# Performance work log

Measured on AMD Instinct MI355X. Metric: run time of the kernel, lower is better.

Reference implementation:

```python
import jax, jax.numpy as jnp
import numpy as np

B, T, D, H = 2, 2048, 1024, 16
HD = D // H  # head_dim = 64

def setup_inputs() -> dict:
    key = jax.random.key(0)
    ks = jax.random.split(key, 6)
    s = 1.0 / np.sqrt(D)
    return {
        "x": jax.random.normal(ks[0], (B, T, D), jnp.float32),
        "Wq": jax.random.normal(ks[1], (D, D), jnp.float32) * s,
        "Wk": jax.random.normal(ks[2], (D, D), jnp.float32) * s,
        "Wv": jax.random.normal(ks[3], (D, D), jnp.float32) * s,
        "Wo": jax.random.normal(ks[4], (D, D), jnp.float32) * s,
        "bo": jnp.zeros((D,), jnp.float32),
    }

def reference(x, Wq, Wk, Wv, Wo, bo):
    b, n, _ = x.shape
    # projections -> [b, h, n, hd]
    def split_heads(t):
        return t.reshape(b, n, H, HD).transpose(0, 2, 1, 3)
    q = split_heads(x @ Wq)
    k = split_heads(x @ Wk)
    v = split_heads(x @ Wv)
    scale = HD ** 0.5
    scores = jnp.einsum('bhqd,bhkd->bhqk', q, k) / scale
    causal = jnp.tril(jnp.ones((n, n), bool))  # True = keep
    scores = jnp.where(causal, scores, -jnp.inf)
    attn = jax.nn.softmax(scores, axis=-1)
    ctx = jnp.einsum('bhqk,bhkd->bhqd', attn, v)
    ctx = ctx.transpose(0, 2, 1, 3).reshape(b, n, D)
    return ctx @ Wo + bo
```

## Files before the change

kernel.cpp:

```cpp
#include <hip/hip_runtime.h>
#include <stdint.h>

typedef unsigned short u16;
typedef unsigned int   u32;
typedef __attribute__((ext_vector_type(8))) __bf16 bf8;
typedef __attribute__((ext_vector_type(4))) float  f4;

#define NEG_INF (-__builtin_inff())

#define BB 2
#define TT 2048
#define DD 1024
#define HH 16
#define HD 64
#define BT (BB*TT)

#define SBAR() __builtin_amdgcn_s_barrier()
#define VMCNT4() asm volatile("s_waitcnt vmcnt(4)" ::: "memory")
#define VMCNT0() asm volatile("s_waitcnt vmcnt(0)" ::: "memory")
#define LGKMCNT0() asm volatile("s_waitcnt lgkmcnt(0)" ::: "memory")

__device__ __forceinline__ u16 f2bf(float f) {
  u32 u = __builtin_bit_cast(u32, f);
  u += 0x7FFFu + ((u >> 16) & 1u);
  return (u16)(u >> 16);
}

__device__ __forceinline__ float exp2fast(float x) {
  float r; asm("v_exp_f32 %0, %1" : "=v"(r) : "v"(x)); return r;
}

__device__ __forceinline__ void g2l16(const void* g, void* l) {
  __builtin_amdgcn_global_load_lds((const __attribute__((address_space(1))) u32*)g,
                                   (__attribute__((address_space(3))) u32*)l, 16, 0, 0);
}

__global__ void k_cast_x(const float* __restrict__ x, uint4* __restrict__ xb) {
  int i = blockIdx.x * 256 + threadIdx.x;
  const float4* xf = (const float4*)x;
  float4 a = xf[2*i], b = xf[2*i+1];
  uint4 o;
  o.x = (u32)f2bf(a.x) | ((u32)f2bf(a.y) << 16);
  o.y = (u32)f2bf(a.z) | ((u32)f2bf(a.w) << 16);
  o.z = (u32)f2bf(b.x) | ((u32)f2bf(b.y) << 16);
  o.w = (u32)f2bf(b.z) | ((u32)f2bf(b.w) << 16);
  xb[i] = o;
}

__global__ void k_twcast(const float* __restrict__ w0, const float* __restrict__ w1,
                         const float* __restrict__ w2, const float* __restrict__ w3,
                         u16* __restrict__ o0, u16* __restrict__ o1,
                         u16* __restrict__ o2, u16* __restrict__ o3) {
  const float* W; u16* O;
  switch (blockIdx.z) {
    case 0: W = w0; O = o0; break;
    case 1: W = w1; O = o1; break;
    case 2: W = w2; O = o2; break;
    default: W = w3; O = o3; break;
  }
  __shared__ __align__(16) u16 tile[64][80];
  int tid = threadIdx.x;
  int k0 = blockIdx.y * 64, n0 = blockIdx.x * 64;
#pragma unroll
  for (int it = 0; it < 4; ++it) {
    int c = it*256 + tid; int kr = c >> 4, ns = c & 15;
    float4 v = *(const float4*)(W + (size_t)(k0+kr)*DD + n0 + ns*4);
    u16* p = &tile[kr][ns*4];
    p[0] = f2bf(v.x); p[1] = f2bf(v.y); p[2] = f2bf(v.z); p[3] = f2bf(v.w);
  }
  __syncthreads();
#pragma unroll
  for (int it = 0; it < 2; ++it) {
    int c = it*256 + tid; int nr = c >> 3, ks = c & 7;
    u32 ww[4];
#pragma unroll
    for (int e = 0; e < 4; ++e) {
      u16 lo = tile[ks*8 + 2*e][nr], hi = tile[ks*8 + 2*e + 1][nr];
      ww[e] = (u32)lo | ((u32)hi << 16);
    }
    uint4 o; o.x = ww[0]; o.y = ww[1]; o.z = ww[2]; o.w = ww[3];
    *(uint4*)(O + (size_t)(n0+nr)*DD + k0 + ks*8) = o;
  }
}

__global__ __launch_bounds__(256, 2) void k_qkv(const u16* __restrict__ xb,
    const u16* __restrict__ wqt, const u16* __restrict__ wkt, const u16* __restrict__ wvt,
    u16* __restrict__ qo, u16* __restrict__ ko, u16* __restrict__ vo) {
  __shared__ __align__(16) char smem[32768];
  int tid = threadIdx.x, w = tid >> 6, l = tid & 63;
  int bid = blockIdx.y * 24 + blockIdx.x;
  int wg = (bid & 7) * 96 + (bid >> 3);
  int nb = wg % 24, mb = wg / 24;
  const u16* Bt = (nb < 8) ? wqt : (nb < 16 ? wkt : wvt);
  int nbl = nb & 7;
  int wm = w >> 1, wn = w & 1;
  f4 z = {0.f, 0.f, 0.f, 0.f};
  f4 acc[4][4];
#pragma unroll
  for (int i = 0; i < 4; ++i)
#pragma unroll
    for (int j = 0; j < 4; ++j) acc[i][j] = z;

  auto stage = [&](int buf, int kt) {
    int kk = kt * 32;
    char* dst = smem + buf * 16384;
#pragma unroll
    for (int i = 0; i < 2; ++i) {
      int c = i*256 + tid; int row = c >> 2, u = c & 3, s = u ^ ((row >> 1) & 3);
      g2l16(xb + (size_t)(mb*128 + row)*DD + kk + s*8, dst + (i*256 + w*64)*16);
    }
#pragma unroll
    for (int i = 0; i < 2; ++i) {
      int c = i*256 + tid; int row = c >> 2, u = c & 3, s = u ^ ((row >> 1) & 3);
      g2l16(Bt + (size_t)(nbl*128 + row)*DD + kk + s*8, dst + 8192 + (i*256 + w*64)*16);
    }
  };

  stage(0, 0);
  VMCNT0(); SBAR();
#pragma unroll 2
  for (int kt = 0; kt < 32; ++kt) {
    int cur = kt & 1;
    if (kt < 31) stage(cur ^ 1, kt + 1);
    char* buf = smem + cur * 16384;
    bf8 af[4], bfr[4];
#pragma unroll
    for (int mf = 0; mf < 4; ++mf) {
      int row = wm*64 + mf*16 + (l & 15);
      int s = (l >> 4) ^ ((row >> 1) & 3);
      af[mf] = *(const bf8*)(buf + row*64 + s*16);
    }
#pragma unroll
    for (int nf = 0; nf < 4; ++nf) {
      int row = wn*64 + nf*16 + (l & 15);
      int s = (l >> 4) ^ ((row >> 1) & 3);
      bfr[nf] = *(const bf8*)(buf + 8192 + row*64 + s*16);
    }
    __builtin_amdgcn_s_setprio(1);
#pragma unroll
    for (int mf = 0; mf < 4; ++mf)
#pragma unroll
      for (int nf = 0; nf < 4; ++nf)
        acc[mf][nf] = __builtin_amdgcn_mfma_f32_16x16x32_bf16(af[mf], bfr[nf], acc[mf][nf], 0, 0, 0);
    __builtin_amdgcn_s_setprio(0);
    LGKMCNT0();
    VMCNT0(); SBAR();
  }
  if (nb < 16) {
    u16* Out = (nb < 8) ? qo : ko;
    float qs = (nb < 8) ? 0.18033688011112042f : 1.0f;
#pragma unroll
    for (int mf = 0; mf < 4; ++mf) {
      int m0 = mb*128 + wm*64 + mf*16 + (l >> 4)*4;
      int b = m0 >> 11;
#pragma unroll
      for (int nf = 0; nf < 4; ++nf) {
        int nn = nbl*128 + wn*64 + nf*16 + (l & 15);
        int h = nn >> 6, d = nn & 63;
#pragma unroll
        for (int r = 0; r < 4; ++r) {
          int t = (m0 + r) & 2047;
          Out[(size_t)((b*HH + h)*TT + t)*HD + d] = f2bf(acc[mf][nf][r] * qs);
        }
      }
    }
  } else {
#pragma unroll
    for (int mf = 0; mf < 4; ++mf) {
      int m0 = mb*128 + wm*64 + mf*16 + (l >> 4)*4;
      int b = m0 >> 11, t0 = m0 & 2047;
#pragma unroll
      for (int nf = 0; nf < 4; ++nf) {
        int nn = nbl*128 + wn*64 + nf*16 + (l & 15);
        int h = nn >> 6, d = nn & 63;
        uint2 o;
        o.x = (u32)f2bf(acc[mf][nf][0]) | ((u32)f2bf(acc[mf][nf][1]) << 16);
        o.y = (u32)f2bf(acc[mf][nf][2]) | ((u32)f2bf(acc[mf][nf][3]) << 16);
        *(uint2*)(vo + (size_t)((b*HH + h)*HD + d)*TT + t0) = o;
      }
    }
  }
}

__global__ __launch_bounds__(256, 2) void k_attn(const u16* __restrict__ q,
    const u16* __restrict__ kk, const u16* __restrict__ vt, u16* __restrict__ ctx) {
  __shared__ __align__(16) char smem[50176];
  int tid = threadIdx.x, w = tid >> 6, l = tid & 63;
  int qi = l & 15, g = l >> 4;
  int fid = blockIdx.x;
  int xcd = fid & 7, j = fid >> 3;
  int bh  = xcd * 4 + (j & 3);
  int ip  = j >> 2;
  u32* Pw = (u32*)(smem + 32768) + w * 1088;
  int b = bh >> 4, h = bh & 15;
  int rot2 = 2 * (qi & 7);

  auto stageK = [&](int t) {
#pragma unroll
    for (int i = 0; i < 4; ++i) {
      int c = i*256 + tid; int row = c >> 3, u = c & 7;
      g2l16(kk + (size_t)(bh*TT + t*128 + row)*HD + (u ^ (row & 7))*8,
            smem + (i*256 + w*64)*16);
    }
  };
  auto stageV = [&](int t) {
#pragma unroll
    for (int i = 0; i < 4; ++i) {
      int c = i*256 + tid; int row = c >> 4, u = c & 15;
      g2l16(vt + (size_t)(bh*HD + row)*TT + t*128 + (u ^ (row & 15))*8,
            smem + 16384 + (i*256 + w*64)*16);
    }
  };

  for (int ps = 0; ps < 2; ++ps) {
    int q0 = (ps ? (31 - ip) : ip) * 64;
    int qw = q0 + w * 16;
    int qrow = qw + qi;
    const u16* qbase = q + (size_t)(bh*TT + qrow)*HD + g*8;
    bf8 qf0 = *(const bf8*)(qbase);
    bf8 qf1 = *(const bf8*)(qbase + 32);
    float mreg = NEG_INF, lreg = 0.f;
    f4 z = {0.f, 0.f, 0.f, 0.f};
    f4 acc[4]; acc[0] = z; acc[1] = z; acc[2] = z; acc[3] = z;
    int nt = (q0 >> 7) + 1;
    stageK(0); stageV(0);
    for (int t = 0; t < nt; ++t) {
      bool last = (t == nt - 1);
      VMCNT4();
      SBAR();
      __builtin_amdgcn_s_setprio(1);
      f4 sv[8];
#pragma unroll
      for (int jf = 0; jf < 8; ++jf) {
        f4 s = z;
        int row = jf*16 + qi;
        int s0 = g ^ (row & 7);
        int s1 = (g + 4) ^ (row & 7);
        bf8 b0 = *(const bf8*)(smem + row*128 + s0*16);
        bf8 b1 = *(const bf8*)(smem + row*128 + s1*16);
        s = __builtin_amdgcn_mfma_f32_16x16x32_bf16(b0, qf0, s, 0, 0, 0);
        s = __builtin_amdgcn_mfma_f32_16x16x32_bf16(b1, qf1, s, 0, 0, 0);
        sv[jf] = s;
      }
      __builtin_amdgcn_s_setprio(0);
      LGKMCNT0();
      SBAR();
      if (!last) stageK(t + 1);
      if (t*128 + 127 > qw) {
        int cbase = qrow - t*128 - 4*g;
#pragma unroll
        for (int jf = 0; jf < 8; ++jf)
#pragma unroll
          for (int r = 0; r < 4; ++r)
            if (jf*16 + r > cbase) sv[jf][r] = NEG_INF;
      }
      float mx = NEG_INF;
#pragma unroll
      for (int jf = 0; jf < 8; ++jf)
        mx = fmaxf(mx, fmaxf(fmaxf(sv[jf][0], sv[jf][1]), fmaxf(sv[jf][2], sv[jf][3])));
      mx = fmaxf(mx, __shfl_xor(mx, 16, 64));
      mx = fmaxf(mx, __shfl_xor(mx, 32, 64));
      float mnew = fmaxf(mreg, mx);
      float alpha = exp2fast(mreg - mnew);
      mreg = mnew;
      float rs = 0.f;
#pragma unroll
      for (int jf = 0; jf < 8; ++jf) {
        float p0 = exp2fast(sv[jf][0] - mreg);
        float p1 = exp2fast(sv[jf][1] - mreg);
        float p2 = exp2fast(sv[jf][2] - mreg);
        float p3 = exp2fast(sv[jf][3] - mreg);
        rs += (p0 + p1) + (p2 + p3);
        uint2 pv;
        pv.x = (u32)f2bf(p0) | ((u32)f2bf(p1) << 16);
        pv.y = (u32)f2bf(p2) | ((u32)f2bf(p3) << 16);
        int blk = 2*jf + (g >> 1);
        *(uint2*)(&Pw[qi*68 + 4*((blk + rot2) & 15) + 2*(g & 1)]) = pv;
      }
      rs += __shfl_xor(rs, 16, 64);
      rs += __shfl_xor(rs, 32, 64);
      lreg = lreg * alpha + rs;
#pragma unroll
      for (int df = 0; df < 4; ++df) {
        f4 a = acc[df];
        a[0] *= alpha; a[1] *= alpha; a[2] *= alpha; a[3] *= alpha;
        acc[df] = a;
      }
      if (!last) { VMCNT4(); } else { VMCNT0(); }
      SBAR();
      __builtin_amdgcn_s_setprio(1);
#pragma unroll
      for (int ks = 0; ks < 4; ++ks) {
        bf8 pf = *(const bf8*)(&Pw[qi*68 + 4*(((4*ks + g) + rot2) & 15)]);
#pragma unroll
        for (int df = 0; df < 4; ++df) {
          int row = df*16 + qi;
          int sl = (ks*4 + g) ^ (row & 15);
          bf8 vf = *(const bf8*)(smem + 16384 + row*256 + sl*16);
          acc[df] = __builtin_amdgcn_mfma_f32_16x16x32_bf16(vf, pf, acc[df], 0, 0, 0);
        }
      }
      __builtin_amdgcn_s_setprio(0);
      LGKMCNT0();
      SBAR();
      if (!last) stageV(t + 1);
    }
    float inv = 1.0f / lreg;
    u16* dst = ctx + (size_t)(b*TT + qrow)*DD + h*HD;
#pragma unroll
    for (int df = 0; df < 4; ++df) {
      uint2 o;
      o.x = (u32)f2bf(acc[df][0] * inv) | ((u32)f2bf(acc[df][1] * inv) << 16);
      o.y = (u32)f2bf(acc[df][2] * inv) | ((u32)f2bf(acc[df][3] * inv) << 16);
      *(uint2*)(dst + df*16 + 4*g) = o;
    }
  }
}

__global__ __launch_bounds__(256, 2) void k_out(const u16* __restrict__ ctx,
    const u16* __restrict__ wot, const float* __restrict__ bo, float* __restrict__ out) {
  __shared__ __align__(16) char smem[24576];
  int tid = threadIdx.x, w = tid >> 6, l = tid & 63;
  int bid = blockIdx.x;
  int wg = (bid & 7) * 64 + (bid >> 3);
  int nb = wg % 16, mb = wg / 16;
  int wm = w >> 1, wn = w & 1;
  f4 z = {0.f, 0.f, 0.f, 0.f};
  f4 acc[4][2];
#pragma unroll
  for (int i = 0; i < 4; ++i) { acc[i][0] = z; acc[i][1] = z; }

  auto stage = [&](int buf, int kt) {
    int kk = kt * 32;
    char* dst = smem + buf * 12288;
#pragma unroll
    for (int i = 0; i < 2; ++i) {
      int c = i*256 + tid; int row = c >> 2, u = c & 3, s = u ^ ((row >> 1) & 3);
      g2l16(ctx + (size_t)(mb*128 + row)*DD + kk + s*8, dst + (i*256 + w*64)*16);
    }
    {
      int row = tid >> 2, u = tid & 3, s = u ^ ((row >> 1) & 3);
      g2l16(wot + (size_t)(nb*64 + row)*DD + kk + s*8, dst + 8192 + (w*64)*16);
    }
  };

  stage(0, 0);
  VMCNT0(); SBAR();
#pragma unroll 2
  for (int kt = 0; kt < 32; ++kt) {
    int cur = kt & 1;
    if (kt < 31) stage(cur ^ 1, kt + 1);
    char* buf = smem + cur * 12288;
    bf8 af[4], bfr[2];
#pragma unroll
    for (int mf = 0; mf < 4; ++mf) {
      int row = wm*64 + mf*16 + (l & 15);
      int s = (l >> 4) ^ ((row >> 1) & 3);
      af[mf] = *(const bf8*)(buf + row*64 + s*16);
    }
#pragma unroll
    for (int nf = 0; nf < 2; ++nf) {
      int row = wn*32 + nf*16 + (l & 15);
      int s = (l >> 4) ^ ((row >> 1) & 3);
      bfr[nf] = *(const bf8*)(buf + 8192 + row*64 + s*16);
    }
    __builtin_amdgcn_s_setprio(1);
#pragma unroll
    for (int mf = 0; mf < 4; ++mf)
#pragma unroll
      for (int nf = 0; nf < 2; ++nf)
        acc[mf][nf] = __builtin_amdgcn_mfma_f32_16x16x32_bf16(af[mf], bfr[nf], acc[mf][nf], 0, 0, 0);
    __builtin_amdgcn_s_setprio(0);
    LGKMCNT0();
    VMCNT0(); SBAR();
  }
#pragma unroll
  for (int nf = 0; nf < 2; ++nf) {
    int n = nb*64 + wn*32 + nf*16 + (l & 15);
    float bias = bo[n];
#pragma unroll
    for (int mf = 0; mf < 4; ++mf) {
      int m0 = mb*128 + wm*64 + mf*16 + (l >> 4)*4;
#pragma unroll
      for (int r = 0; r < 4; ++r)
        out[(size_t)(m0 + r)*DD + n] = acc[mf][nf][r] + bias;
    }
  }
}

extern "C" void kernel_launch(void* const* d_in, const int* in_sizes, int n_in,
                              void* d_out, int out_size, void* d_ws, size_t ws_size,
                              hipStream_t stream) {
  const float* x  = (const float*)d_in[0];
  const float* Wq = (const float*)d_in[1];
  const float* Wk = (const float*)d_in[2];
  const float* Wv = (const float*)d_in[3];
  const float* Wo = (const float*)d_in[4];
  const float* bo = (const float*)d_in[5];
  float* out = (float*)d_out;
  char* ws = (char*)d_ws;

  u16* xb  = (u16*)(ws);
  u16* wqt = (u16*)(ws + 8388608);
  u16* wkt = (u16*)(ws + 10485760);
  u16* wvt = (u16*)(ws + 12582912);
  u16* wot = (u16*)(ws + 14680064);
  u16* qb_ = (u16*)(ws + 16777216);
  u16* kb_ = (u16*)(ws + 25165824);
  u16* vtb = (u16*)(ws + 41943040);
  u16* cxb = (u16*)(ws + 50331648);

  k_cast_x<<<dim3(2048), dim3(256), 0, stream>>>(x, (uint4*)xb);
  k_twcast<<<dim3(16, 16, 4), dim3(256), 0, stream>>>(Wq, Wk, Wv, Wo, wqt, wkt, wvt, wot);
  k_qkv<<<dim3(24, 32), dim3(256), 0, stream>>>(xb, wqt, wkt, wvt, qb_, kb_, vtb);
  k_attn<<<dim3(512), dim3(256), 0, stream>>>(qb_, kb_, vtb, cxb);
  k_out<<<dim3(512), dim3(256), 0, stream>>>(cxb, wot, bo, out);
}
```

Measured before the change: 174.7 us.

## Double GEMM K-tile depth, add lazy softmax rescaling, use hardware bf16 packing

The QKV and output-projection GEMMs now stage 64-wide K tiles instead of 32, with a matching 8-way XOR swizzle and twice the shared memory. This halves the number of barrier and wait cycles per tile. The attention kernel skips the running-max rescale of the accumulator and row sum unless some lane's new max exceeds the old one by more than 8 (log2 units), which saves exp and multiply work but lets unnormalised values grow by up to 2^8. Manual bf16 rounding is replaced by a compiler bf16 conversion for P and the context output. The larger LDS footprint may reduce occupancy in the GEMM kernels.

```diff
diff --git a/kernel.cpp b/kernel.cpp
--- a/kernel.cpp
+++ b/kernel.cpp
@@ -4,6 +4,7 @@
 typedef unsigned short u16;
 typedef unsigned int   u32;
 typedef __attribute__((ext_vector_type(8))) __bf16 bf8;
+typedef __attribute__((ext_vector_type(2))) __bf16 bf2;
 typedef __attribute__((ext_vector_type(4))) float  f4;
 
 #define NEG_INF (-__builtin_inff())
@@ -24,6 +25,11 @@
   u32 u = __builtin_bit_cast(u32, f);
   u += 0x7FFFu + ((u >> 16) & 1u);
   return (u16)(u >> 16);
+}
+
+__device__ __forceinline__ u32 pkbf(float a, float b) {
+  bf2 v; v[0] = (__bf16)a; v[1] = (__bf16)b;
+  return __builtin_bit_cast(u32, v);
 }
 
 __device__ __forceinline__ float exp2fast(float x) {
@@ -86,7 +92,7 @@
 __global__ __launch_bounds__(256, 2) void k_qkv(const u16* __restrict__ xb,
     const u16* __restrict__ wqt, const u16* __restrict__ wkt, const u16* __restrict__ wvt,
     u16* __restrict__ qo, u16* __restrict__ ko, u16* __restrict__ vo) {
-  __shared__ __align__(16) char smem[32768];
+  __shared__ __align__(16) char smem[65536];
   int tid = threadIdx.x, w = tid >> 6, l = tid & 63;
   int bid = blockIdx.y * 24 + blockIdx.x;
   int wg = (bid & 7) * 96 + (bid >> 3);
@@ -94,6 +100,7 @@
   const u16* Bt = (nb < 8) ? wqt : (nb < 16 ? wkt : wvt);
   int nbl = nb & 7;
   int wm = w >> 1, wn = w & 1;
+  int qi = l & 15, g = l >> 4;
   f4 z = {0.f, 0.f, 0.f, 0.f};
   f4 acc[4][4];
 #pragma unroll
@@ -102,47 +109,50 @@
     for (int j = 0; j < 4; ++j) acc[i][j] = z;
 
   auto stage = [&](int buf, int kt) {
-    int kk = kt * 32;
-    char* dst = smem + buf * 16384;
-#pragma unroll
-    for (int i = 0; i < 2; ++i) {
-      int c = i*256 + tid; int row = c >> 2, u = c & 3, s = u ^ ((row >> 1) & 3);
+    int kk = kt * 64;
+    char* dst = smem + buf * 32768;
+#pragma unroll
+    for (int i = 0; i < 4; ++i) {
+      int c = i*256 + tid; int row = c >> 3, u = c & 7, s = u ^ (row & 7);
       g2l16(xb + (size_t)(mb*128 + row)*DD + kk + s*8, dst + (i*256 + w*64)*16);
     }
 #pragma unroll
-    for (int i = 0; i < 2; ++i) {
-      int c = i*256 + tid; int row = c >> 2, u = c & 3, s = u ^ ((row >> 1) & 3);
-      g2l16(Bt + (size_t)(nbl*128 + row)*DD + kk + s*8, dst + 8192 + (i*256 + w*64)*16);
+    for (int i = 0; i < 4; ++i) {
+      int c = i*256 + tid; int row = c >> 3, u = c & 7, s = u ^ (row & 7);
+      g2l16(Bt + (size_t)(nbl*128 + row)*DD + kk + s*8, dst + 16384 + (i*256 + w*64)*16);
     }
   };
 
   stage(0, 0);
   VMCNT0(); SBAR();
 #pragma unroll 2
-  for (int kt = 0; kt < 32; ++kt) {
+  for (int kt = 0; kt < 16; ++kt) {
     int cur = kt & 1;
-    if (kt < 31) stage(cur ^ 1, kt + 1);
-    char* buf = smem + cur * 16384;
-    bf8 af[4], bfr[4];
-#pragma unroll
-    for (int mf = 0; mf < 4; ++mf) {
-      int row = wm*64 + mf*16 + (l & 15);
-      int s = (l >> 4) ^ ((row >> 1) & 3);
-      af[mf] = *(const bf8*)(buf + row*64 + s*16);
-    }
-#pragma unroll
-    for (int nf = 0; nf < 4; ++nf) {
-      int row = wn*64 + nf*16 + (l & 15);
-      int s = (l >> 4) ^ ((row >> 1) & 3);
-      bfr[nf] = *(const bf8*)(buf + 8192 + row*64 + s*16);
-    }
-    __builtin_amdgcn_s_setprio(1);
-#pragma unroll
-    for (int mf = 0; mf < 4; ++mf)
-#pragma unroll
-      for (int nf = 0; nf < 4; ++nf)
-        acc[mf][nf] = __builtin_amdgcn_mfma_f32_16x16x32_bf16(af[mf], bfr[nf], acc[mf][nf], 0, 0, 0);
-    __builtin_amdgcn_s_setprio(0);
+    if (kt < 15) stage(cur ^ 1, kt + 1);
+    char* buf = smem + cur * 32768;
+#pragma unroll
+    for (int ks2 = 0; ks2 < 2; ++ks2) {
+      bf8 af[4], bfr[4];
+#pragma unroll
+      for (int mf = 0; mf < 4; ++mf) {
+        int row = wm*64 + mf*16 + qi;
+        int s = (ks2*4 + g) ^ (row & 7);
+        af[mf] = *(const bf8*)(buf + row*128 + s*16);
+      }
+#pragma unroll
+      for (int nf = 0; nf < 4; ++nf) {
+        int row = wn*64 + nf*16 + qi;
+        int s = (ks2*4 + g) ^ (row & 7);
+        bfr[nf] = *(const bf8*)(buf + 16384 + row*128 + s*16);
+      }
+      __builtin_amdgcn_s_setprio(1);
+#pragma unroll
+      for (int mf = 0; mf < 4; ++mf)
+#pragma unroll
+        for (int nf = 0; nf < 4; ++nf)
+          acc[mf][nf] = __builtin_amdgcn_mfma_f32_16x16x32_bf16(af[mf], bfr[nf], acc[mf][nf], 0, 0, 0);
+      __builtin_amdgcn_s_setprio(0);
+    }
     LGKMCNT0();
     VMCNT0(); SBAR();
   }
@@ -151,11 +161,11 @@
     float qs = (nb < 8) ? 0.18033688011112042f : 1.0f;
 #pragma unroll
     for (int mf = 0; mf < 4; ++mf) {
-      int m0 = mb*128 + wm*64 + mf*16 + (l >> 4)*4;
+      int m0 = mb*128 + wm*64 + mf*16 + g*4;
       int b = m0 >> 11;
 #pragma unroll
       for (int nf = 0; nf < 4; ++nf) {
-        int nn = nbl*128 + wn*64 + nf*16 + (l & 15);
+        int nn = nbl*128 + wn*64 + nf*16 + qi;
         int h = nn >> 6, d = nn & 63;
 #pragma unroll
         for (int r = 0; r < 4; ++r) {
@@ -167,11 +177,11 @@
   } else {
 #pragma unroll
     for (int mf = 0; mf < 4; ++mf) {
-      int m0 = mb*128 + wm*64 + mf*16 + (l >> 4)*4;
+      int m0 = mb*128 + wm*64 + mf*16 + g*4;
       int b = m0 >> 11, t0 = m0 & 2047;
 #pragma unroll
       for (int nf = 0; nf < 4; ++nf) {
-        int nn = nbl*128 + wn*64 + nf*16 + (l & 15);
+        int nn = nbl*128 + wn*64 + nf*16 + qi;
         int h = nn >> 6, d = nn & 63;
         uint2 o;
         o.x = (u32)f2bf(acc[mf][nf][0]) | ((u32)f2bf(acc[mf][nf][1]) << 16);
@@ -260,9 +270,18 @@
         mx = fmaxf(mx, fmaxf(fmaxf(sv[jf][0], sv[jf][1]), fmaxf(sv[jf][2], sv[jf][3])));
       mx = fmaxf(mx, __shfl_xor(mx, 16, 64));
       mx = fmaxf(mx, __shfl_xor(mx, 32, 64));
-      float mnew = fmaxf(mreg, mx);
-      float alpha = exp2fast(mreg - mnew);
-      mreg = mnew;
+      if (!__all(mx <= mreg + 8.f)) {
+        float mnew = fmaxf(mreg, mx);
+        float alpha = exp2fast(mreg - mnew);
+        mreg = mnew;
+        lreg *= alpha;
+#pragma unroll
+        for (int df = 0; df < 4; ++df) {
+          f4 a = acc[df];
+          a[0] *= alpha; a[1] *= alpha; a[2] *= alpha; a[3] *= alpha;
+          acc[df] = a;
+        }
+      }
       float rs = 0.f;
 #pragma unroll
       for (int jf = 0; jf < 8; ++jf) {
@@ -272,20 +291,14 @@
         float p3 = exp2fast(sv[jf][3] - mreg);
         rs += (p0 + p1) + (p2 + p3);
         uint2 pv;
-        pv.x = (u32)f2bf(p0) | ((u32)f2bf(p1) << 16);
-        pv.y = (u32)f2bf(p2) | ((u32)f2bf(p3) << 16);
+        pv.x = pkbf(p0, p1);
+        pv.y = pkbf(p2, p3);
         int blk = 2*jf + (g >> 1);
         *(uint2*)(&Pw[qi*68 + 4*((blk + rot2) & 15) + 2*(g & 1)]) = pv;
       }
       rs += __shfl_xor(rs, 16, 64);
       rs += __shfl_xor(rs, 32, 64);
-      lreg = lreg * alpha + rs;
-#pragma unroll
-      for (int df = 0; df < 4; ++df) {
-        f4 a = acc[df];
-        a[0] *= alpha; a[1] *= alpha; a[2] *= alpha; a[3] *= alpha;
-        acc[df] = a;
-      }
+      lreg += rs;
       if (!last) { VMCNT4(); } else { VMCNT0(); }
       SBAR();
       __builtin_amdgcn_s_setprio(1);
@@ -310,8 +323,8 @@
 #pragma unroll
     for (int df = 0; df < 4; ++df) {
       uint2 o;
-      o.x = (u32)f2bf(acc[df][0] * inv) | ((u32)f2bf(acc[df][1] * inv) << 16);
-      o.y = (u32)f2bf(acc[df][2] * inv) | ((u32)f2bf(acc[df][3] * inv) << 16);
+      o.x = pkbf(acc[df][0] * inv, acc[df][1] * inv);
+      o.y = pkbf(acc[df][2] * inv, acc[df][3] * inv);
       *(uint2*)(dst + df*16 + 4*g) = o;
     }
   }
@@ -319,68 +332,73 @@
 
 __global__ __launch_bounds__(256, 2) void k_out(const u16* __restrict__ ctx,
     const u16* __restrict__ wot, const float* __restrict__ bo, float* __restrict__ out) {
-  __shared__ __align__(16) char smem[24576];
+  __shared__ __align__(16) char smem[49152];
   int tid = threadIdx.x, w = tid >> 6, l = tid & 63;
   int bid = blockIdx.x;
   int wg = (bid & 7) * 64 + (bid >> 3);
   int nb = wg % 16, mb = wg / 16;
   int wm = w >> 1, wn = w & 1;
+  int qi = l & 15, g = l >> 4;
   f4 z = {0.f, 0.f, 0.f, 0.f};
   f4 acc[4][2];
 #pragma unroll
   for (int i = 0; i < 4; ++i) { acc[i][0] = z; acc[i][1] = z; }
 
   auto stage = [&](int buf, int kt) {
-    int kk = kt * 32;
-    char* dst = smem + buf * 12288;
+    int kk = kt * 64;
+    char* dst = smem + buf * 24576;
+#pragma unroll
+    for (int i = 0; i < 4; ++i) {
+      int c = i*256 + tid; int row = c >> 3, u = c & 7, s = u ^ (row & 7);
+      g2l16(ctx + (size_t)(mb*128 + row)*DD + kk + s*8, dst + (i*256 + w*64)*16);
+    }
 #pragma unroll
     for (int i = 0; i < 2; ++i) {
-      int c = i*256 + tid; int row = c >> 2, u = c & 3, s = u ^ ((row >> 1) & 3);
-      g2l16(ctx + (size_t)(mb*128 + row)*DD + kk + s*8, dst + (i*256 + w*64)*16);
-    }
-    {
-      int row = tid >> 2, u = tid & 3, s = u ^ ((row >> 1) & 3);
-      g2l16(wot + (size_t)(nb*64 + row)*DD + kk + s*8, dst + 8192 + (w*64)*16);
+      int c = i*256 + tid; int row = c >> 3, u = c & 7, s = u ^ (row & 7);
+      g2l16(wot + (size_t)(nb*64 + row)*DD + kk + s*8, dst + 16384 + (i*256 + w*64)*16);
     }
   };
 
   stage(0, 0);
   VMCNT0(); SBAR();
 #pragma unroll 2
-  for (int kt = 0; kt < 32; ++kt) {
+  for (int kt = 0; kt < 16; ++kt) {
     int cur = kt & 1;
-    if (kt < 31) stage(cur ^ 1, kt + 1);
-    char* buf = smem + cur * 12288;
-    bf8 af[4], bfr[2];
-#pragma unroll
-    for (int mf = 0; mf < 4; ++mf) {
-      int row = wm*64 + mf*16 + (l & 15);
-      int s = (l >> 4) ^ ((row >> 1) & 3);
-      af[mf] = *(const bf8*)(buf + row*64 + s*16);
-    }
-#pragma unroll
-    for (int nf = 0; nf < 2; ++nf) {
-      int row = wn*32 + nf*16 + (l & 15);
-      int s = (l >> 4) ^ ((row >> 1) & 3);
-      bfr[nf] = *(const bf8*)(buf + 8192 + row*64 + s*16);
-    }
-    __builtin_amdgcn_s_setprio(1);
-#pragma unroll
-    for (int mf = 0; mf < 4; ++mf)
-#pragma unroll
-      for (int nf = 0; nf < 2; ++nf)
-        acc[mf][nf] = __builtin_amdgcn_mfma_f32_16x16x32_bf16(af[mf], bfr[nf], acc[mf][nf], 0, 0, 0);
-    __builtin_amdgcn_s_setprio(0);
+    if (kt < 15) stage(cur ^ 1, kt + 1);
+    char* buf = smem + cur * 24576;
+#pragma unroll
+    for (int ks2 = 0; ks2 < 2; ++ks2) {
+      bf8 af[4], bfr[2];
+#pragma unroll
+      for (int mf = 0; mf < 4; ++mf) {
+        int row = wm*64 + mf*16 + qi;
+        int s = (ks2*4 + g) ^ (row & 7);
+        af[mf] = *(const bf8*)(buf + row*128 + s*16);
+      }
+#pragma unroll
+      for (int nf = 0; nf < 2; ++nf) {
+        int row = wn*32 + nf*16 + qi;
+        int s = (ks2*4 + g) ^ (row & 7);
+        bfr[nf] = *(const bf8*)(buf + 16384 + row*128 + s*16);
+      }
+      __builtin_amdgcn_s_setprio(1);
+#pragma unroll
+      for (int mf = 0; mf < 4; ++mf)
+#pragma unroll
+        for (int nf = 0; nf < 2; ++nf)
+          acc[mf][nf] = __builtin_amdgcn_mfma_f32_16x16x32_bf16(af[mf], bfr[nf], acc[mf][nf], 0, 0, 0);
+      __builtin_amdgcn_s_setprio(0);
+    }
     LGKMCNT0();
     VMCNT0(); SBAR();
   }
 #pragma unroll
   for (int nf = 0; nf < 2; ++nf) {
-    int n = nb*64 + wn*32 + nf*16 + (l & 15);
+    int n = nb*64 + wn*32 + nf*16 + qi;
     float bias = bo[n];
 #pragma unroll
     for (int mf = 0; mf < 4; ++mf) {
-      int m0 = mb*128 + wm*64 + mf*16 + (l >> 4)*4;
+      int m0 = mb*128 + wm*64 + mf*16 + g*4;
 #pragma unroll
       for (int r = 0; r < 4; ++r)
         out[(size_t)(m0 + r)*DD + n] = acc[mf][nf][r] + bias;
```

Result: faster. 166.6 us (-4.6%).
